# Performance work log

Hardware: AMD Instinct MI355X
Metric: run time of the kernel (lower is better)

Reference implementation:

```python
import jax, jax.numpy as jnp
import numpy as np
import math

B, H, S, D = 4, 16, 1024, 64
NEG = -1000000000.0

def setup_inputs() -> dict:
    key = jax.random.key(0)
    ks = jax.random.split(key, 6)
    return {
        "query": jax.random.normal(ks[0], (B, H, S, D), dtype=jnp.float32),
        "key": jax.random.normal(ks[1], (B, H, S, D), dtype=jnp.float32),
        "value": jax.random.normal(ks[2], (B, H, S, D), dtype=jnp.float32),
        "head_nums": H,
        "mask": jax.random.randint(ks[3], (B, S), 0, 2, dtype=jnp.int32),
        "topic_query": jax.random.normal(ks[4], (B, S, D), dtype=jnp.float32),
        "topic_key": jax.random.normal(ks[5], (B, S, D), dtype=jnp.float32),
    }

def reference(query, key, value, head_nums, mask, topic_query, topic_key):
    d = query.shape[-1]
    # scores: [B,H,S,S]
    scores = jnp.einsum("bhqd,bhkd->bhqk", query, key) / math.sqrt(d)
    # pairwise mask: [B,S,S] (mask_i * mask_j)
    pair_mask = (mask[:, :, None] * mask[:, None, :]) != 0
    scores = jnp.where(pair_mask[:, None, :, :], scores, NEG)
    # topic modulation: per-token (no head dim), broadcast over heads
    dt = topic_query.shape[-1]
    topic_scores = jnp.einsum("bqd,bkd->bqk", topic_query, topic_key) / math.sqrt(dt)
    topic_scores = jnp.where(pair_mask, topic_scores, 1.0)[:, None, :, :]  # [B,1,S,S]
    topic_probs = jax.nn.softmax(topic_scores, axis=-1)
    scores = scores * topic_probs
    p_attn = jax.nn.softmax(scores, axis=-1)
    out = jnp.einsum("bhqk,bhkd->bhqd", p_attn, value)
    return (out, p_attn)
```

## Files before the change

### kernel.cpp

```cpp
#include <hip/hip_runtime.h>

#define B_ 4
#define H_ 16
#define S_ 1024
#define D_ 64
#define NEGV -1000000000.0f

typedef __bf16 bf16x8 __attribute__((ext_vector_type(8)));
typedef __bf16 bf16x4 __attribute__((ext_vector_type(4)));
typedef float f32x4 __attribute__((ext_vector_type(4)));

#define MFMA16(A, B, C) __builtin_amdgcn_mfma_f32_16x16x32_bf16(A, B, C, 0, 0, 0)

__device__ __forceinline__ void bar_lds() {
  asm volatile("s_waitcnt lgkmcnt(0)" ::: "memory");
  __builtin_amdgcn_sched_barrier(0);
  __builtin_amdgcn_s_barrier();
  __builtin_amdgcn_sched_barrier(0);
}

__device__ __forceinline__ bf16x8 cvt8(const float* p) {
  float4 x = *(const float4*)p;
  float4 y = *(const float4*)(p + 4);
  bf16x8 f;
  f[0]=(__bf16)x.x; f[1]=(__bf16)x.y; f[2]=(__bf16)x.z; f[3]=(__bf16)x.w;
  f[4]=(__bf16)y.x; f[5]=(__bf16)y.y; f[6]=(__bf16)y.z; f[7]=(__bf16)y.w;
  return f;
}

__global__ __launch_bounds__(256) void prep_kernel(
    const float* __restrict__ K, const float* __restrict__ V,
    __bf16* __restrict__ Kb, __bf16* __restrict__ Vt)
{
  int bid = blockIdx.x;
  int sc = bid & 15;
  int bh = bid >> 4;
  int tid = threadIdx.x;
  __shared__ float s_v[64][65];

  const float* Kc = K + ((size_t)bh*S_ + sc*64)*D_;
  const float* Vc = V + ((size_t)bh*S_ + sc*64)*D_;
  __bf16* Kbc = Kb + ((size_t)bh*S_ + sc*64)*D_;

  {
    const float4* src = (const float4*)Kc + tid*4;
    float4 a = src[0], b = src[1], c = src[2], d = src[3];
    bf16x8 o0, o1;
    o0[0]=(__bf16)a.x; o0[1]=(__bf16)a.y; o0[2]=(__bf16)a.z; o0[3]=(__bf16)a.w;
    o0[4]=(__bf16)b.x; o0[5]=(__bf16)b.y; o0[6]=(__bf16)b.z; o0[7]=(__bf16)b.w;
    o1[0]=(__bf16)c.x; o1[1]=(__bf16)c.y; o1[2]=(__bf16)c.z; o1[3]=(__bf16)c.w;
    o1[4]=(__bf16)d.x; o1[5]=(__bf16)d.y; o1[6]=(__bf16)d.z; o1[7]=(__bf16)d.w;
    *(bf16x8*)(Kbc + tid*16)     = o0;
    *(bf16x8*)(Kbc + tid*16 + 8) = o1;
  }
  for (int i = tid; i < 64*16; i += 256) {
    int r = i >> 4, c4 = i & 15;
    float4 v = ((const float4*)(Vc + (size_t)r*D_))[c4];
    s_v[r][c4*4+0] = v.x; s_v[r][c4*4+1] = v.y;
    s_v[r][c4*4+2] = v.z; s_v[r][c4*4+3] = v.w;
  }
  __syncthreads();
  {
    int d = tid >> 2, seg = tid & 3;
    bf16x8 o0, o1;
    #pragma unroll
    for (int j = 0; j < 8; ++j) o0[j] = (__bf16)s_v[seg*16 + j][d];
    #pragma unroll
    for (int j = 0; j < 8; ++j) o1[j] = (__bf16)s_v[seg*16 + 8 + j][d];
    __bf16* dst = Vt + ((size_t)bh*D_ + d)*S_ + sc*64 + seg*16;
    *(bf16x8*)dst = o0;
    *(bf16x8*)(dst + 8) = o1;
  }
}

__global__ __launch_bounds__(256) void topic_kernel(
    const float* __restrict__ tq, const float* __restrict__ tk,
    const int* __restrict__ mask, __bf16* __restrict__ tp)
{
  int bid0 = blockIdx.x;
  int bid = (bid0 & 7)*32 + (bid0 >> 3);
  int qt = bid & 63, b = bid >> 6;
  int tid = threadIdx.x, wave = tid >> 6, lane = tid & 63;
  int l15 = lane & 15, lhi = lane >> 4;
  __shared__ float2 s_red[4][16];
  __shared__ __align__(16) char s_mem[4*8704];

  const int* mb = mask + b*S_;
  bf16x8 qf[2];
  #pragma unroll
  for (int dc = 0; dc < 2; ++dc)
    qf[dc] = cvt8(tq + ((size_t)b*S_ + qt*16 + l15)*D_ + dc*32 + lhi*8);
  int mq = mb[qt*16 + l15];

  f32x4 sc[16];
  #pragma unroll
  for (int kt = 0; kt < 16; ++kt) {
    int kb = wave*256 + kt*16;
    const float* kr = tk + ((size_t)b*S_ + kb + l15)*D_ + lhi*8;
    bf16x8 k0 = cvt8(kr);
    bf16x8 k1 = cvt8(kr + 32);
    f32x4 acc = {0.f,0.f,0.f,0.f};
    acc = MFMA16(k0, qf[0], acc);
    acc = MFMA16(k1, qf[1], acc);
    int4 mk = *(const int4*)(mb + kb + lhi*4);
    sc[kt][0] = (mq && mk.x) ? acc[0]*0.125f : 1.0f;
    sc[kt][1] = (mq && mk.y) ? acc[1]*0.125f : 1.0f;
    sc[kt][2] = (mq && mk.z) ? acc[2]*0.125f : 1.0f;
    sc[kt][3] = (mq && mk.w) ? acc[3]*0.125f : 1.0f;
  }
  float m = -3.4e38f;
  #pragma unroll
  for (int kt = 0; kt < 16; ++kt)
    #pragma unroll
    for (int i = 0; i < 4; ++i) m = fmaxf(m, sc[kt][i]);
  m = fmaxf(m, __shfl_xor(m, 16));
  m = fmaxf(m, __shfl_xor(m, 32));
  float sum = 0.f;
  #pragma unroll
  for (int kt = 0; kt < 16; ++kt)
    #pragma unroll
    for (int i = 0; i < 4; ++i) { sc[kt][i] = __expf(sc[kt][i] - m); sum += sc[kt][i]; }
  sum += __shfl_xor(sum, 16);
  sum += __shfl_xor(sum, 32);
  if (lane < 16) s_red[wave][l15] = make_float2(m, sum);
  bar_lds();
  float M = -3.4e38f;
  #pragma unroll
  for (int w = 0; w < 4; ++w) M = fmaxf(M, s_red[w][l15].x);
  float Z = 0.f;
  #pragma unroll
  for (int w = 0; w < 4; ++w) Z += s_red[w][l15].y * __expf(s_red[w][l15].x - M);
  float scale = __expf(m - M) / Z;

  #pragma unroll
  for (int kt = 0; kt < 16; ++kt) {
    int kb = wave*256 + kt*16;
    int4 mk = *(const int4*)(mb + kb + lhi*4);
    sc[kt][0] *= scale; if (!(mq && mk.x)) sc[kt][0] = -sc[kt][0];
    sc[kt][1] *= scale; if (!(mq && mk.y)) sc[kt][1] = -sc[kt][1];
    sc[kt][2] *= scale; if (!(mq && mk.z)) sc[kt][2] = -sc[kt][2];
    sc[kt][3] *= scale; if (!(mq && mk.w)) sc[kt][3] = -sc[kt][3];
  }

  float* xw = (float*)s_mem + wave*2176;
  __bf16* tpw = tp + ((size_t)b*S_ + qt*16)*S_ + wave*256;
  #pragma unroll
  for (int h = 0; h < 2; ++h) {
    #pragma unroll
    for (int j = 0; j < 8; ++j)
      *(f32x4*)(xw + l15*136 + j*16 + lhi*4) = sc[h*8 + j];
    bar_lds();
    #pragma unroll
    for (int rr = 0; rr < 8; ++rr) {
      int r = rr*2 + (lane >> 5);
      f32x4 a = *(f32x4*)(xw + r*136 + (lane & 31)*4);
      bf16x4 o;
      o[0]=(__bf16)a[0]; o[1]=(__bf16)a[1]; o[2]=(__bf16)a[2]; o[3]=(__bf16)a[3];
      *(bf16x4*)(tpw + (size_t)r*S_ + h*128 + (lane & 31)*4) = o;
    }
    bar_lds();
  }
}

__global__ __launch_bounds__(256) void attn_kernel(
    const float* __restrict__ Q, const __bf16* __restrict__ Kb,
    const __bf16* __restrict__ Vt, const __bf16* __restrict__ tp,
    float* __restrict__ out, float* __restrict__ pa)
{
  int bid0 = blockIdx.x;
  int bid = (bid0 & 7)*512 + (bid0 >> 3);
  int qt = bid & 63;
  int h  = (bid >> 6) & 15;
  int b  = bid >> 10;
  int tid = threadIdx.x, wave = tid >> 6, lane = tid & 63;
  int l15 = lane & 15, lhi = lane >> 4;

  __shared__ __align__(16) char s_mem[17408];
  __shared__ float2 s_red[4][16];

  size_t bh = (size_t)b*H_ + h;
  const __bf16* Kbh = Kb + bh*S_*D_;
  const __bf16* tpb = tp + ((size_t)b*S_ + qt*16 + l15)*S_;

  bf16x8 qf[2];
  #pragma unroll
  for (int dc = 0; dc < 2; ++dc)
    qf[dc] = cvt8(Q + (bh*S_ + qt*16 + l15)*D_ + dc*32 + lhi*8);

  bf16x4 sb[16];
  bf16x8 rk0[2], rk1[2];
  bf16x4 rt[2];
  {
    const __bf16* kr = Kbh + (size_t)(wave*256 + l15)*D_ + lhi*8;
    rk0[0] = *(const bf16x8*)kr;
    rk1[0] = *(const bf16x8*)(kr + 32);
    rt[0]  = *(const bf16x4*)(tpb + wave*256 + lhi*4);
  }
  #pragma unroll
  for (int kt = 0; kt < 16; ++kt) {
    const int cur = kt & 1;
    if (kt < 15) {
      const int nxt = cur ^ 1;
      int kb = wave*256 + (kt+1)*16;
      const __bf16* kr = Kbh + (size_t)(kb + l15)*D_ + lhi*8;
      rk0[nxt] = *(const bf16x8*)kr;
      rk1[nxt] = *(const bf16x8*)(kr + 32);
      rt[nxt]  = *(const bf16x4*)(tpb + kb + lhi*4);
    }
    f32x4 acc = {0.f,0.f,0.f,0.f};
    acc = MFMA16(rk0[cur], qf[0], acc);
    acc = MFMA16(rk1[cur], qf[1], acc);
    #pragma unroll
    for (int i = 0; i < 4; ++i) {
      float t = (float)rt[cur][i];
      float s = (t > 0.f) ? acc[i]*0.125f*t : NEGV*(-t);
      sb[kt][i] = (__bf16)s;
    }
  }

  float m = -3.4e38f;
  #pragma unroll
  for (int kt = 0; kt < 16; ++kt)
    #pragma unroll
    for (int i = 0; i < 4; ++i) m = fmaxf(m, (float)sb[kt][i]);
  m = fmaxf(m, __shfl_xor(m, 16));
  m = fmaxf(m, __shfl_xor(m, 32));
  float sum = 0.f;
  #pragma unroll
  for (int kt = 0; kt < 16; ++kt)
    #pragma unroll
    for (int i = 0; i < 4; ++i) sum += __expf((float)sb[kt][i] - m);
  sum += __shfl_xor(sum, 16);
  sum += __shfl_xor(sum, 32);
  if (lane < 16) s_red[wave][l15] = make_float2(m, sum);
  bar_lds();
  float M = -3.4e38f;
  #pragma unroll
  for (int w = 0; w < 4; ++w) M = fmaxf(M, s_red[w][l15].x);
  float Z = 0.f;
  #pragma unroll
  for (int w = 0; w < 4; ++w) Z += s_red[w][l15].y * __expf(s_red[w][l15].x - M);
  const float scale = __expf(m - M) / Z;
  bar_lds();

  float* xw = (float*)s_mem + wave*4352/4;
  float* paw = pa + (bh*S_ + qt*16)*S_ + wave*256;
  #pragma unroll
  for (int hh = 0; hh < 4; ++hh) {
    #pragma unroll
    for (int j = 0; j < 4; ++j) {
      int kt = hh*4 + j;
      f32x4 pv;
      #pragma unroll
      for (int i = 0; i < 4; ++i) pv[i] = __expf((float)sb[kt][i] - m) * scale;
      *(f32x4*)(xw + l15*68 + j*16 + lhi*4) = pv;
    }
    bar_lds();
    #pragma unroll
    for (int rr = 0; rr < 4; ++rr) {
      int r = rr*4 + lhi;
      f32x4 a = *(f32x4*)(xw + r*68 + l15*4);
      __builtin_nontemporal_store(a, (f32x4*)(paw + (size_t)r*S_ + hh*64 + l15*4));
    }
    bar_lds();
  }

  const __bf16* Vh = Vt + (bh*D_ + wave*16 + l15)*S_ + lhi*8;
  f32x4 oacc = {0.f,0.f,0.f,0.f};
  #pragma unroll
  for (int h2 = 0; h2 < 2; ++h2) {
    if ((wave >> 1) == h2) {
      int cb = (wave & 1)*256;
      #pragma unroll
      for (int kt = 0; kt < 16; ++kt) {
        bf16x4 pb;
        #pragma unroll
        for (int i = 0; i < 4; ++i) pb[i] = (__bf16)(__expf((float)sb[kt][i] - m) * scale);
        int col = cb + kt*16 + lhi*4;
        *(bf16x4*)(s_mem + l15*1024 + ((col*2) ^ ((l15 & 7) << 4))) = pb;
      }
    }
    bar_lds();
    #pragma unroll
    for (int ks = 0; ks < 16; ++ks) {
      bf16x8 a  = *(const bf16x8*)(s_mem + l15*1024 + ((ks*64 + lhi*16) ^ ((l15 & 7) << 4)));
      bf16x8 bv = *(const bf16x8*)(Vh + h2*512 + ks*32);
      oacc = MFMA16(a, bv, oacc);
    }
    bar_lds();
  }
  #pragma unroll
  for (int i = 0; i < 4; ++i)
    __builtin_nontemporal_store(oacc[i], out + (bh*S_ + qt*16 + lhi*4 + i)*D_ + wave*16 + l15);
}

extern "C" void kernel_launch(void* const* d_in, const int* in_sizes, int n_in,
                              void* d_out, int out_size, void* d_ws, size_t ws_size,
                              hipStream_t stream) {
  const float* Q    = (const float*)d_in[0];
  const float* K    = (const float*)d_in[1];
  const float* V    = (const float*)d_in[2];
  const int*   mask = (const int*)d_in[4];
  const float* tq   = (const float*)d_in[5];
  const float* tk   = (const float*)d_in[6];

  __bf16* tp = (__bf16*)d_ws;
  __bf16* Kb = tp + (size_t)B_*S_*S_;
  __bf16* Vt = Kb + (size_t)B_*H_*S_*D_;

  float* outp = (float*)d_out;
  float* pa   = outp + (size_t)B_*H_*S_*D_;

  prep_kernel <<<B_*H_*16, 256, 0, stream>>>(K, V, Kb, Vt);
  topic_kernel<<<B_*64,    256, 0, stream>>>(tq, tk, mask, tp);
  attn_kernel <<<B_*H_*64, 256, 0, stream>>>(Q, Kb, Vt, tp, outp, pa);
}
```

Before: 189.9 us.

## Restructure attention to single-wave blocks with online softmax and score recompute

Each block now uses one wave that computes the row max and sum with an online softmax over all keys, then recomputes the scores to write probabilities and accumulate PV. This removes the cross-wave LDS reduction, the block barriers and the large shared staging buffer, which frees LDS and raises occupancy. In exchange QK^T and the topic loads are done twice and each wave handles four times more keys serially.

```diff
diff --git a/kernel.cpp b/kernel.cpp
--- a/kernel.cpp
+++ b/kernel.cpp
@@ -162,7 +162,7 @@
   }
 }
 
-__global__ __launch_bounds__(256) void attn_kernel(
+__global__ __launch_bounds__(64) void attn_kernel(
     const float* __restrict__ Q, const __bf16* __restrict__ Kb,
     const __bf16* __restrict__ Vt, const __bf16* __restrict__ tp,
     float* __restrict__ out, float* __restrict__ pa)
@@ -172,126 +172,111 @@
   int qt = bid & 63;
   int h  = (bid >> 6) & 15;
   int b  = bid >> 10;
-  int tid = threadIdx.x, wave = tid >> 6, lane = tid & 63;
+  int lane = threadIdx.x;
   int l15 = lane & 15, lhi = lane >> 4;
 
-  __shared__ __align__(16) char s_mem[17408];
-  __shared__ float2 s_red[4][16];
+  __shared__ __align__(16) char s_mem[16*68*4 + 16*36*2];
+  float*  scr = (float*)s_mem;
+  __bf16* bnc = (__bf16*)(s_mem + 16*68*4);
 
   size_t bh = (size_t)b*H_ + h;
   const __bf16* Kbh = Kb + bh*S_*D_;
+  const __bf16* Vth = Vt + bh*D_*S_;
   const __bf16* tpb = tp + ((size_t)b*S_ + qt*16 + l15)*S_;
 
-  bf16x8 qf[2];
-  #pragma unroll
-  for (int dc = 0; dc < 2; ++dc)
-    qf[dc] = cvt8(Q + (bh*S_ + qt*16 + l15)*D_ + dc*32 + lhi*8);
-
-  bf16x4 sb[16];
-  bf16x8 rk0[2], rk1[2];
-  bf16x4 rt[2];
+  bf16x8 qf0 = cvt8(Q + (bh*S_ + qt*16 + l15)*D_ + lhi*8);
+  bf16x8 qf1 = cvt8(Q + (bh*S_ + qt*16 + l15)*D_ + 32 + lhi*8);
+
+  float mr = -3.4e38f, zr = 0.f;
+  #pragma unroll 4
+  for (int kt = 0; kt < 64; ++kt) {
+    const __bf16* kr = Kbh + (size_t)(kt*16 + l15)*D_ + lhi*8;
+    bf16x8 k0 = *(const bf16x8*)kr;
+    bf16x8 k1 = *(const bf16x8*)(kr + 32);
+    bf16x4 t  = *(const bf16x4*)(tpb + kt*16 + lhi*4);
+    f32x4 acc = {0.f,0.f,0.f,0.f};
+    acc = MFMA16(k0, qf0, acc);
+    acc = MFMA16(k1, qf1, acc);
+    f32x4 s;
+    #pragma unroll
+    for (int i = 0; i < 4; ++i) {
+      float tv = (float)t[i];
+      s[i] = (tv > 0.f) ? acc[i]*0.125f*tv : NEGV*(-tv);
+    }
+    float nm = fmaxf(fmaxf(fmaxf(s[0], s[1]), fmaxf(s[2], s[3])), mr);
+    zr = zr*__expf(mr - nm)
+       + __expf(s[0]-nm) + __expf(s[1]-nm) + __expf(s[2]-nm) + __expf(s[3]-nm);
+    mr = nm;
+  }
   {
-    const __bf16* kr = Kbh + (size_t)(wave*256 + l15)*D_ + lhi*8;
-    rk0[0] = *(const bf16x8*)kr;
-    rk1[0] = *(const bf16x8*)(kr + 32);
-    rt[0]  = *(const bf16x4*)(tpb + wave*256 + lhi*4);
-  }
-  #pragma unroll
-  for (int kt = 0; kt < 16; ++kt) {
-    const int cur = kt & 1;
-    if (kt < 15) {
-      const int nxt = cur ^ 1;
-      int kb = wave*256 + (kt+1)*16;
-      const __bf16* kr = Kbh + (size_t)(kb + l15)*D_ + lhi*8;
-      rk0[nxt] = *(const bf16x8*)kr;
-      rk1[nxt] = *(const bf16x8*)(kr + 32);
-      rt[nxt]  = *(const bf16x4*)(tpb + kb + lhi*4);
+    float mo = __shfl_xor(mr, 16);
+    float zo = __shfl_xor(zr, 16);
+    float nm = fmaxf(mr, mo);
+    zr = zr*__expf(mr-nm) + zo*__expf(mo-nm);
+    mr = nm;
+    mo = __shfl_xor(mr, 32);
+    zo = __shfl_xor(zr, 32);
+    nm = fmaxf(mr, mo);
+    zr = zr*__expf(mr-nm) + zo*__expf(mo-nm);
+    mr = nm;
+  }
+  const float invZ = 1.f / zr;
+
+  f32x4 o0 = {0,0,0,0}, o1 = {0,0,0,0}, o2 = {0,0,0,0}, o3 = {0,0,0,0};
+  float* paw = pa + (bh*S_ + qt*16)*S_;
+
+  for (int cp = 0; cp < 16; ++cp) {
+    #pragma unroll
+    for (int half = 0; half < 2; ++half) {
+      int c = cp*2 + half;
+      #pragma unroll
+      for (int j = 0; j < 2; ++j) {
+        int kt = c*2 + j;
+        const __bf16* kr = Kbh + (size_t)(kt*16 + l15)*D_ + lhi*8;
+        bf16x8 k0 = *(const bf16x8*)kr;
+        bf16x8 k1 = *(const bf16x8*)(kr + 32);
+        bf16x4 t  = *(const bf16x4*)(tpb + kt*16 + lhi*4);
+        f32x4 acc = {0.f,0.f,0.f,0.f};
+        acc = MFMA16(k0, qf0, acc);
+        acc = MFMA16(k1, qf1, acc);
+        f32x4 p;
+        #pragma unroll
+        for (int i = 0; i < 4; ++i) {
+          float tv = (float)t[i];
+          float s = (tv > 0.f) ? acc[i]*0.125f*tv : NEGV*(-tv);
+          p[i] = __expf(s - mr) * invZ;
+        }
+        *(f32x4*)(scr + l15*68 + half*32 + j*16 + lhi*4) = p;
+        bf16x4 pb;
+        pb[0]=(__bf16)p[0]; pb[1]=(__bf16)p[1]; pb[2]=(__bf16)p[2]; pb[3]=(__bf16)p[3];
+        *(bf16x4*)(bnc + l15*36 + j*16 + lhi*4) = pb;
+      }
+      asm volatile("s_waitcnt lgkmcnt(0)" ::: "memory");
+      bf16x8 A = *(const bf16x8*)(bnc + l15*36 + lhi*8);
+      const __bf16* Vb = Vth + (size_t)l15*S_ + c*32 + lhi*8;
+      o0 = MFMA16(A, *(const bf16x8*)(Vb          ), o0);
+      o1 = MFMA16(A, *(const bf16x8*)(Vb + 16*S_  ), o1);
+      o2 = MFMA16(A, *(const bf16x8*)(Vb + 32*S_  ), o2);
+      o3 = MFMA16(A, *(const bf16x8*)(Vb + 48*S_  ), o3);
     }
-    f32x4 acc = {0.f,0.f,0.f,0.f};
-    acc = MFMA16(rk0[cur], qf[0], acc);
-    acc = MFMA16(rk1[cur], qf[1], acc);
-    #pragma unroll
-    for (int i = 0; i < 4; ++i) {
-      float t = (float)rt[cur][i];
-      float s = (t > 0.f) ? acc[i]*0.125f*t : NEGV*(-t);
-      sb[kt][i] = (__bf16)s;
-    }
-  }
-
-  float m = -3.4e38f;
-  #pragma unroll
-  for (int kt = 0; kt < 16; ++kt)
-    #pragma unroll
-    for (int i = 0; i < 4; ++i) m = fmaxf(m, (float)sb[kt][i]);
-  m = fmaxf(m, __shfl_xor(m, 16));
-  m = fmaxf(m, __shfl_xor(m, 32));
-  float sum = 0.f;
-  #pragma unroll
-  for (int kt = 0; kt < 16; ++kt)
-    #pragma unroll
-    for (int i = 0; i < 4; ++i) sum += __expf((float)sb[kt][i] - m);
-  sum += __shfl_xor(sum, 16);
-  sum += __shfl_xor(sum, 32);
-  if (lane < 16) s_red[wave][l15] = make_float2(m, sum);
-  bar_lds();
-  float M = -3.4e38f;
-  #pragma unroll
-  for (int w = 0; w < 4; ++w) M = fmaxf(M, s_red[w][l15].x);
-  float Z = 0.f;
-  #pragma unroll
-  for (int w = 0; w < 4; ++w) Z += s_red[w][l15].y * __expf(s_red[w][l15].x - M);
-  const float scale = __expf(m - M) / Z;
-  bar_lds();
-
-  float* xw = (float*)s_mem + wave*4352/4;
-  float* paw = pa + (bh*S_ + qt*16)*S_ + wave*256;
-  #pragma unroll
-  for (int hh = 0; hh < 4; ++hh) {
-    #pragma unroll
-    for (int j = 0; j < 4; ++j) {
-      int kt = hh*4 + j;
-      f32x4 pv;
-      #pragma unroll
-      for (int i = 0; i < 4; ++i) pv[i] = __expf((float)sb[kt][i] - m) * scale;
-      *(f32x4*)(xw + l15*68 + j*16 + lhi*4) = pv;
-    }
-    bar_lds();
+    asm volatile("s_waitcnt lgkmcnt(0)" ::: "memory");
     #pragma unroll
     for (int rr = 0; rr < 4; ++rr) {
       int r = rr*4 + lhi;
-      f32x4 a = *(f32x4*)(xw + r*68 + l15*4);
-      __builtin_nontemporal_store(a, (f32x4*)(paw + (size_t)r*S_ + hh*64 + l15*4));
+      f32x4 a = *(const f32x4*)(scr + r*68 + l15*4);
+      __builtin_nontemporal_store(a, (f32x4*)(paw + (size_t)r*S_ + cp*64 + l15*4));
     }
-    bar_lds();
-  }
-
-  const __bf16* Vh = Vt + (bh*D_ + wave*16 + l15)*S_ + lhi*8;
-  f32x4 oacc = {0.f,0.f,0.f,0.f};
-  #pragma unroll
-  for (int h2 = 0; h2 < 2; ++h2) {
-    if ((wave >> 1) == h2) {
-      int cb = (wave & 1)*256;
-      #pragma unroll
-      for (int kt = 0; kt < 16; ++kt) {
-        bf16x4 pb;
-        #pragma unroll
-        for (int i = 0; i < 4; ++i) pb[i] = (__bf16)(__expf((float)sb[kt][i] - m) * scale);
-        int col = cb + kt*16 + lhi*4;
-        *(bf16x4*)(s_mem + l15*1024 + ((col*2) ^ ((l15 & 7) << 4))) = pb;
-      }
-    }
-    bar_lds();
-    #pragma unroll
-    for (int ks = 0; ks < 16; ++ks) {
-      bf16x8 a  = *(const bf16x8*)(s_mem + l15*1024 + ((ks*64 + lhi*16) ^ ((l15 & 7) << 4)));
-      bf16x8 bv = *(const bf16x8*)(Vh + h2*512 + ks*32);
-      oacc = MFMA16(a, bv, oacc);
-    }
-    bar_lds();
-  }
-  #pragma unroll
-  for (int i = 0; i < 4; ++i)
-    __builtin_nontemporal_store(oacc[i], out + (bh*S_ + qt*16 + lhi*4 + i)*D_ + wave*16 + l15);
+    asm volatile("s_waitcnt lgkmcnt(0)" ::: "memory");
+  }
+
+  #pragma unroll
+  for (int i = 0; i < 4; ++i) {
+    float* orow = out + (bh*S_ + qt*16 + lhi*4 + i)*D_ + l15;
+    __builtin_nontemporal_store(o0[i], orow);
+    __builtin_nontemporal_store(o1[i], orow + 16);
+    __builtin_nontemporal_store(o2[i], orow + 32);
+    __builtin_nontemporal_store(o3[i], orow + 48);
+  }
 }
 
 extern "C" void kernel_launch(void* const* d_in, const int* in_sizes, int n_in,
@@ -313,5 +298,5 @@
 
   prep_kernel <<<B_*H_*16, 256, 0, stream>>>(K, V, Kb, Vt);
   topic_kernel<<<B_*64,    256, 0, stream>>>(tq, tk, mask, tp);
-  attn_kernel <<<B_*H_*64, 256, 0, stream>>>(Q, Kb, Vt, tp, outp, pa);
-}
+  attn_kernel <<<B_*H_*64, 64, 0, stream>>>(Q, Kb, Vt, tp, outp, pa);
+}
```

Result: slower. 263.0 us (+38.5%).

## Fuse P-store and PV MFMA per wave, reduce partial outputs across waves

Applied to the files above, without the earlier changes.

Each wave now computes its own slice of the P·V product directly from its 256 key columns, staging probabilities through a small per-wave LDS scratch. That scratch feeds both the coalesced p_attn stores and the bf16 MFMA A operand, which removes the block-wide barriers and the two-phase P buffer. Partial outputs from the four waves are then summed through LDS before the final store. In exchange the work adds an LDS reduction and issues four MFMAs per 32-key chunk, with V loads spread across all waves.

```diff
diff --git a/kernel.cpp b/kernel.cpp
--- a/kernel.cpp
+++ b/kernel.cpp
@@ -175,17 +175,17 @@
   int tid = threadIdx.x, wave = tid >> 6, lane = tid & 63;
   int l15 = lane & 15, lhi = lane >> 4;
 
-  __shared__ __align__(16) char s_mem[17408];
+  __shared__ __align__(16) float s_scr[4][16][36];
+  __shared__ __align__(16) float s_out[4][16][64];
   __shared__ float2 s_red[4][16];
 
   size_t bh = (size_t)b*H_ + h;
   const __bf16* Kbh = Kb + bh*S_*D_;
+  const __bf16* Vth = Vt + bh*D_*S_;
   const __bf16* tpb = tp + ((size_t)b*S_ + qt*16 + l15)*S_;
 
-  bf16x8 qf[2];
-  #pragma unroll
-  for (int dc = 0; dc < 2; ++dc)
-    qf[dc] = cvt8(Q + (bh*S_ + qt*16 + l15)*D_ + dc*32 + lhi*8);
+  bf16x8 qf0 = cvt8(Q + (bh*S_ + qt*16 + l15)*D_ + lhi*8);
+  bf16x8 qf1 = cvt8(Q + (bh*S_ + qt*16 + l15)*D_ + 32 + lhi*8);
 
   bf16x4 sb[16];
   bf16x8 rk0[2], rk1[2];
@@ -208,8 +208,8 @@
       rt[nxt]  = *(const bf16x4*)(tpb + kb + lhi*4);
     }
     f32x4 acc = {0.f,0.f,0.f,0.f};
-    acc = MFMA16(rk0[cur], qf[0], acc);
-    acc = MFMA16(rk1[cur], qf[1], acc);
+    acc = MFMA16(rk0[cur], qf0, acc);
+    acc = MFMA16(rk1[cur], qf1, acc);
     #pragma unroll
     for (int i = 0; i < 4; ++i) {
       float t = (float)rt[cur][i];
@@ -241,57 +241,61 @@
   #pragma unroll
   for (int w = 0; w < 4; ++w) Z += s_red[w][l15].y * __expf(s_red[w][l15].x - M);
   const float scale = __expf(m - M) / Z;
+
+  f32x4 o0 = {0,0,0,0}, o1 = {0,0,0,0}, o2 = {0,0,0,0}, o3 = {0,0,0,0};
+  float* paw = pa + (bh*S_ + qt*16)*S_ + wave*256;
+  #pragma unroll 2
+  for (int c = 0; c < 8; ++c) {
+    #pragma unroll
+    for (int j = 0; j < 2; ++j) {
+      int kt = c*2 + j;
+      f32x4 p;
+      #pragma unroll
+      for (int i = 0; i < 4; ++i) p[i] = __expf((float)sb[kt][i] - m) * scale;
+      *(f32x4*)&s_scr[wave][l15][j*16 + lhi*4] = p;
+    }
+    asm volatile("s_waitcnt lgkmcnt(0)" ::: "memory");
+    __builtin_amdgcn_sched_barrier(0);
+    {
+      int r = lhi*4 + (l15 >> 2), col = (l15 & 3)*8;
+      f32x4 a0 = *(const f32x4*)&s_scr[wave][r][col];
+      f32x4 a1 = *(const f32x4*)&s_scr[wave][r][col+4];
+      float* dst = paw + (size_t)r*S_ + c*32 + col;
+      __builtin_nontemporal_store(a0, (f32x4*)dst);
+      __builtin_nontemporal_store(a1, (f32x4*)(dst+4));
+    }
+    bf16x8 A;
+    {
+      f32x4 a0 = *(const f32x4*)&s_scr[wave][l15][lhi*8];
+      f32x4 a1 = *(const f32x4*)&s_scr[wave][l15][lhi*8+4];
+      A[0]=(__bf16)a0[0]; A[1]=(__bf16)a0[1]; A[2]=(__bf16)a0[2]; A[3]=(__bf16)a0[3];
+      A[4]=(__bf16)a1[0]; A[5]=(__bf16)a1[1]; A[6]=(__bf16)a1[2]; A[7]=(__bf16)a1[3];
+    }
+    const __bf16* Vb = Vth + (size_t)l15*S_ + wave*256 + c*32 + lhi*8;
+    o0 = MFMA16(A, *(const bf16x8*)(Vb        ), o0);
+    o1 = MFMA16(A, *(const bf16x8*)(Vb + 16*S_), o1);
+    o2 = MFMA16(A, *(const bf16x8*)(Vb + 32*S_), o2);
+    o3 = MFMA16(A, *(const bf16x8*)(Vb + 48*S_), o3);
+  }
+
+  #pragma unroll
+  for (int i = 0; i < 4; ++i) {
+    int q = lhi*4 + i;
+    s_out[wave][q][l15]      = o0[i];
+    s_out[wave][q][l15 + 16] = o1[i];
+    s_out[wave][q][l15 + 32] = o2[i];
+    s_out[wave][q][l15 + 48] = o3[i];
+  }
   bar_lds();
-
-  float* xw = (float*)s_mem + wave*4352/4;
-  float* paw = pa + (bh*S_ + qt*16)*S_ + wave*256;
-  #pragma unroll
-  for (int hh = 0; hh < 4; ++hh) {
-    #pragma unroll
-    for (int j = 0; j < 4; ++j) {
-      int kt = hh*4 + j;
-      f32x4 pv;
-      #pragma unroll
-      for (int i = 0; i < 4; ++i) pv[i] = __expf((float)sb[kt][i] - m) * scale;
-      *(f32x4*)(xw + l15*68 + j*16 + lhi*4) = pv;
-    }
-    bar_lds();
-    #pragma unroll
-    for (int rr = 0; rr < 4; ++rr) {
-      int r = rr*4 + lhi;
-      f32x4 a = *(f32x4*)(xw + r*68 + l15*4);
-      __builtin_nontemporal_store(a, (f32x4*)(paw + (size_t)r*S_ + hh*64 + l15*4));
-    }
-    bar_lds();
-  }
-
-  const __bf16* Vh = Vt + (bh*D_ + wave*16 + l15)*S_ + lhi*8;
-  f32x4 oacc = {0.f,0.f,0.f,0.f};
-  #pragma unroll
-  for (int h2 = 0; h2 < 2; ++h2) {
-    if ((wave >> 1) == h2) {
-      int cb = (wave & 1)*256;
-      #pragma unroll
-      for (int kt = 0; kt < 16; ++kt) {
-        bf16x4 pb;
-        #pragma unroll
-        for (int i = 0; i < 4; ++i) pb[i] = (__bf16)(__expf((float)sb[kt][i] - m) * scale);
-        int col = cb + kt*16 + lhi*4;
-        *(bf16x4*)(s_mem + l15*1024 + ((col*2) ^ ((l15 & 7) << 4))) = pb;
-      }
-    }
-    bar_lds();
-    #pragma unroll
-    for (int ks = 0; ks < 16; ++ks) {
-      bf16x8 a  = *(const bf16x8*)(s_mem + l15*1024 + ((ks*64 + lhi*16) ^ ((l15 & 7) << 4)));
-      bf16x8 bv = *(const bf16x8*)(Vh + h2*512 + ks*32);
-      oacc = MFMA16(a, bv, oacc);
-    }
-    bar_lds();
-  }
-  #pragma unroll
-  for (int i = 0; i < 4; ++i)
-    __builtin_nontemporal_store(oacc[i], out + (bh*S_ + qt*16 + lhi*4 + i)*D_ + wave*16 + l15);
+  {
+    int q = tid >> 4, d = (tid & 15)*4;
+    f32x4 s0 = *(const f32x4*)&s_out[0][q][d];
+    f32x4 s1 = *(const f32x4*)&s_out[1][q][d];
+    f32x4 s2 = *(const f32x4*)&s_out[2][q][d];
+    f32x4 s3 = *(const f32x4*)&s_out[3][q][d];
+    f32x4 r = (s0 + s1) + (s2 + s3);
+    __builtin_nontemporal_store(r, (f32x4*)(out + (bh*S_ + qt*16 + q)*D_ + d));
+  }
 }
 
 extern "C" void kernel_launch(void* const* d_in, const int* in_sizes, int n_in,
```

Result: slower. 319.5 us (+68.2%).
